# Kernel optimization log

Measured on AMD Instinct MI355X. Metric: run time of the kernel, lower is better.

The kernel has to match this reference:

```python
import jax, jax.numpy as jnp
import numpy as np

B, T, U = 4, 448, 448
SKS, BKS, H, V = 96, 32, 96, 128


def setup_inputs() -> dict:
    key = jax.random.key(0)
    ks = jax.random.split(key, 8)
    return {
        "s": jax.random.normal(ks[0], (B, T, SKS), jnp.float32),
        "b": jax.random.normal(ks[1], (B, U, BKS), jnp.float32),
        "W_sh": jax.random.normal(ks[2], (H, SKS), jnp.float32) * (1.0 / np.sqrt(SKS)),
        "b_sh": jax.random.normal(ks[3], (H,), jnp.float32) * 0.02,
        "W_bh": jax.random.normal(ks[4], (H, BKS), jnp.float32) * (1.0 / np.sqrt(BKS)),
        "b_bh": jax.random.normal(ks[5], (H,), jnp.float32) * 0.02,
        "W_out": jax.random.normal(ks[6], (V, H), jnp.float32) * (1.0 / np.sqrt(H)),
        "b_out": jax.random.normal(ks[7], (V,), jnp.float32) * 0.02,
    }


def reference(s, b, W_sh, b_sh, W_bh, b_bh, W_out, b_out):
    # input projections (self.sh / self.bh): [B,T,H] and [B,U,H]
    sh = jnp.einsum("bts,hs->bth", s, W_sh) + b_sh
    bh = jnp.einsum("buk,hk->buh", b, W_bh) + b_bh
    # broadcast outer-expand + relu gate: z[b,t,u,h] = sh[b,t,h] * relu(bh[b,u,h])
    z = sh[:, :, None, :] * jax.nn.relu(bh)[:, None, :, :]  # [B,T,U,H]
    # output projection (self.out) + log_softmax over vocab
    logits = jnp.einsum("btuh,vh->btuv", z, W_out) + b_out  # [B,T,U,V]
    return jax.nn.log_softmax(logits, axis=-1)
```

## Files before the change

kernel.cpp:

```cpp
#include <hip/hip_runtime.h>

#define B_ 4
#define T_ 448
#define U_ 448
#define SKS_ 96
#define BKS_ 32
#define H_ 96
#define V_ 128

typedef __attribute__((ext_vector_type(8))) short bf16x8;
typedef __attribute__((ext_vector_type(4))) float f32x4;
typedef __attribute__((ext_vector_type(4))) int i32x4;

__device__ __forceinline__ unsigned short f2bf(float f) {
    unsigned int u = __float_as_uint(f);
    u += 0x7fffu + ((u >> 16) & 1u);
    return (unsigned short)(u >> 16);
}
__device__ __forceinline__ float bf2f(unsigned short h) {
    return __uint_as_float(((unsigned int)h) << 16);
}

__global__ __launch_bounds__(128) void prep_kernel(
    const float* __restrict__ s, const float* __restrict__ b,
    const float* __restrict__ W_sh, const float* __restrict__ b_sh,
    const float* __restrict__ W_bh, const float* __restrict__ b_bh,
    const float* __restrict__ W_out,
    unsigned short* __restrict__ sh_ws,
    unsigned short* __restrict__ rbh_ws,
    unsigned short* __restrict__ w_ws)
{
    const int blk = blockIdx.x;
    const int tid = threadIdx.x;

    if (blk < B_ * T_) {
        __shared__ float row[SKS_];
        if (tid < SKS_) row[tid] = s[(size_t)blk * SKS_ + tid];
        __syncthreads();
        if (tid < H_) {
            const float* w = W_sh + (size_t)tid * SKS_;
            float acc = b_sh[tid];
            #pragma unroll
            for (int k = 0; k < SKS_; k += 4) {
                acc += row[k] * w[k] + row[k + 1] * w[k + 1]
                     + row[k + 2] * w[k + 2] + row[k + 3] * w[k + 3];
            }
            sh_ws[(size_t)blk * H_ + tid] = f2bf(acc);
        }
    } else if (blk < 2 * B_ * T_) {
        const int r = blk - B_ * T_;
        __shared__ float row2[BKS_];
        if (tid < BKS_) row2[tid] = b[(size_t)r * BKS_ + tid];
        __syncthreads();
        if (tid < H_) {
            const float* w = W_bh + (size_t)tid * BKS_;
            float acc = b_bh[tid];
            #pragma unroll
            for (int k = 0; k < BKS_; k += 4) {
                acc += row2[k] * w[k] + row2[k + 1] * w[k + 1]
                     + row2[k + 2] * w[k + 2] + row2[k + 3] * w[k + 3];
            }
            acc = fmaxf(acc, 0.0f);
            rbh_ws[(size_t)r * H_ + tid] = f2bf(acc);
        }
    } else {
        const int c = (blk - 2 * B_ * T_) * 128 + tid;
        const int k8 = c >> 7;
        const int n  = c & 127;
        const float* src = W_out + (size_t)n * H_ + k8 * 8;
        unsigned short tmp[8];
        #pragma unroll
        for (int j = 0; j < 8; j++) tmp[j] = f2bf(src[j]);
        i32x4 v;
        v.x = (int)((unsigned)tmp[0] | ((unsigned)tmp[1] << 16));
        v.y = (int)((unsigned)tmp[2] | ((unsigned)tmp[3] << 16));
        v.z = (int)((unsigned)tmp[4] | ((unsigned)tmp[5] << 16));
        v.w = (int)((unsigned)tmp[6] | ((unsigned)tmp[7] << 16));
        ((i32x4*)w_ws)[c] = v;
    }
}

__global__ __launch_bounds__(256) void joiner_kernel(
    const unsigned short* __restrict__ sh_ws,
    const unsigned short* __restrict__ rbh_ws,
    const unsigned short* __restrict__ w_ws,
    const float* __restrict__ b_out,
    float* __restrict__ out)
{
    __shared__ unsigned short Wl[12 * 128 * 8];
    __shared__ unsigned short Al[12 * 16 * 8];

    const int tid = threadIdx.x;
    const int u0  = blockIdx.x * 16;
    const int t0  = blockIdx.y * 4;
    const int bb  = blockIdx.z;

    {
        const i32x4* src = (const i32x4*)w_ws;
        i32x4* dst = (i32x4*)Wl;
        #pragma unroll
        for (int i = 0; i < 6; i++) {
            const int c = i * 256 + tid;
            dst[c] = src[c];
        }
    }
    if (tid < 192) {
        const int u  = tid & 15;
        const int k8 = tid >> 4;
        const i32x4* src = (const i32x4*)(rbh_ws +
            ((size_t)(bb * U_ + u0 + u)) * H_ + k8 * 8);
        ((i32x4*)Al)[tid] = *src;
    }
    __syncthreads();

    const int wave = tid >> 6;
    const int lane = tid & 63;
    const int t    = t0 + wave;
    const int n    = lane & 15;
    const int q    = lane >> 4;

    const unsigned short* shrow = sh_ws + ((size_t)(bb * T_ + t)) * H_;
    bf16x8 shf[3];
    #pragma unroll
    for (int ks = 0; ks < 3; ks++)
        shf[ks] = *(const bf16x8*)(shrow + ks * 32 + q * 8);

    f32x4 acc[8];
    #pragma unroll
    for (int nt = 0; nt < 8; nt++) acc[nt] = (f32x4){0.f, 0.f, 0.f, 0.f};

    #pragma unroll
    for (int ks = 0; ks < 3; ks++) {
        const bf16x8 rb = *(const bf16x8*)(Al + (ks * 64 + lane) * 8);
        bf16x8 af;
        #pragma unroll
        for (int j = 0; j < 8; j++) {
            const float z = bf2f((unsigned short)shf[ks][j]) *
                            bf2f((unsigned short)rb[j]);
            af[j] = (short)f2bf(z);
        }
        #pragma unroll
        for (int nt = 0; nt < 8; nt++) {
            const bf16x8 bfr = *(const bf16x8*)(Wl +
                ((size_t)((ks * 4 + q) * 128 + nt * 16 + n)) * 8);
            acc[nt] = __builtin_amdgcn_mfma_f32_16x16x32_bf16(af, bfr, acc[nt], 0, 0, 0);
        }
    }

    float bias[8];
    #pragma unroll
    for (int nt = 0; nt < 8; nt++) bias[nt] = b_out[nt * 16 + n];

    #pragma unroll
    for (int nt = 0; nt < 8; nt++) {
        #pragma unroll
        for (int r = 0; r < 4; r++) acc[nt][r] += bias[nt];
    }

    #pragma unroll
    for (int r = 0; r < 4; r++) {
        float m = acc[0][r];
        #pragma unroll
        for (int nt = 1; nt < 8; nt++) m = fmaxf(m, acc[nt][r]);
        #pragma unroll
        for (int sft = 1; sft <= 8; sft <<= 1)
            m = fmaxf(m, __shfl_xor(m, sft, 64));

        float ssum = 0.0f;
        #pragma unroll
        for (int nt = 0; nt < 8; nt++) ssum += __expf(acc[nt][r] - m);
        #pragma unroll
        for (int sft = 1; sft <= 8; sft <<= 1)
            ssum += __shfl_xor(ssum, sft, 64);

        const float logz = m + __logf(ssum);
        const int u_local = q * 4 + r;
        float* orow = out + (((size_t)(bb * T_ + t)) * U_ + (u0 + u_local)) * V_;
        #pragma unroll
        for (int nt = 0; nt < 8; nt++)
            orow[nt * 16 + n] = acc[nt][r] - logz;
    }
}

extern "C" void kernel_launch(void* const* d_in, const int* in_sizes, int n_in,
                              void* d_out, int out_size, void* d_ws, size_t ws_size,
                              hipStream_t stream)
{
    const float* s     = (const float*)d_in[0];
    const float* b     = (const float*)d_in[1];
    const float* W_sh  = (const float*)d_in[2];
    const float* b_sh  = (const float*)d_in[3];
    const float* W_bh  = (const float*)d_in[4];
    const float* b_bh  = (const float*)d_in[5];
    const float* W_out = (const float*)d_in[6];
    const float* b_out = (const float*)d_in[7];
    float* out = (float*)d_out;

    unsigned short* sh_ws  = (unsigned short*)d_ws;
    unsigned short* rbh_ws = sh_ws + (size_t)B_ * T_ * H_;
    unsigned short* w_ws   = rbh_ws + (size_t)B_ * U_ * H_;

    prep_kernel<<<2 * B_ * T_ + 12, 128, 0, stream>>>(
        s, b, W_sh, b_sh, W_bh, b_bh, W_out, sh_ws, rbh_ws, w_ws);

    joiner_kernel<<<dim3(U_ / 16, T_ / 4, B_), 256, 0, stream>>>(
        sh_ws, rbh_ws, w_ws, b_out, out);
}
```

Before: 425.8 us.

## Use MFMA for input projections and loop multiple t-rows per joiner block

```diff
diff --git a/kernel.cpp b/kernel.cpp
--- a/kernel.cpp
+++ b/kernel.cpp
@@ -20,8 +20,18 @@
 __device__ __forceinline__ float bf2f(unsigned short h) {
     return __uint_as_float(((unsigned int)h) << 16);
 }
-
-__global__ __launch_bounds__(128) void prep_kernel(
+__device__ __forceinline__ bf16x8 load_cvt8(const float* __restrict__ p) {
+    f32x4 a = *(const f32x4*)p;
+    f32x4 c = *(const f32x4*)(p + 4);
+    bf16x8 r;
+    r[0] = (short)f2bf(a.x); r[1] = (short)f2bf(a.y);
+    r[2] = (short)f2bf(a.z); r[3] = (short)f2bf(a.w);
+    r[4] = (short)f2bf(c.x); r[5] = (short)f2bf(c.y);
+    r[6] = (short)f2bf(c.z); r[7] = (short)f2bf(c.w);
+    return r;
+}
+
+__global__ __launch_bounds__(256) void prep_kernel(
     const float* __restrict__ s, const float* __restrict__ b,
     const float* __restrict__ W_sh, const float* __restrict__ b_sh,
     const float* __restrict__ W_bh, const float* __restrict__ b_bh,
@@ -30,44 +40,64 @@
     unsigned short* __restrict__ rbh_ws,
     unsigned short* __restrict__ w_ws)
 {
-    const int blk = blockIdx.x;
-    const int tid = threadIdx.x;
-
-    if (blk < B_ * T_) {
-        __shared__ float row[SKS_];
-        if (tid < SKS_) row[tid] = s[(size_t)blk * SKS_ + tid];
-        __syncthreads();
-        if (tid < H_) {
-            const float* w = W_sh + (size_t)tid * SKS_;
-            float acc = b_sh[tid];
-            #pragma unroll
-            for (int k = 0; k < SKS_; k += 4) {
-                acc += row[k] * w[k] + row[k + 1] * w[k + 1]
-                     + row[k + 2] * w[k + 2] + row[k + 3] * w[k + 3];
-            }
-            sh_ws[(size_t)blk * H_ + tid] = f2bf(acc);
-        }
-    } else if (blk < 2 * B_ * T_) {
-        const int r = blk - B_ * T_;
-        __shared__ float row2[BKS_];
-        if (tid < BKS_) row2[tid] = b[(size_t)r * BKS_ + tid];
-        __syncthreads();
-        if (tid < H_) {
-            const float* w = W_bh + (size_t)tid * BKS_;
-            float acc = b_bh[tid];
-            #pragma unroll
-            for (int k = 0; k < BKS_; k += 4) {
-                acc += row2[k] * w[k] + row2[k + 1] * w[k + 1]
-                     + row2[k + 2] * w[k + 2] + row2[k + 3] * w[k + 3];
-            }
-            acc = fmaxf(acc, 0.0f);
-            rbh_ws[(size_t)r * H_ + tid] = f2bf(acc);
+    const int blk  = blockIdx.x;
+    const int tid  = threadIdx.x;
+    const int wave = tid >> 6;
+    const int lane = tid & 63;
+    const int n    = lane & 15;
+    const int q    = lane >> 4;
+
+    if (blk < 28) {
+        const int row0 = blk * 64 + wave * 16;
+        bf16x8 af[3];
+        #pragma unroll
+        for (int ks = 0; ks < 3; ks++)
+            af[ks] = load_cvt8(s + (size_t)(row0 + n) * SKS_ + ks * 32 + q * 8);
+        f32x4 acc[6];
+        #pragma unroll
+        for (int nt = 0; nt < 6; nt++) acc[nt] = (f32x4){0.f, 0.f, 0.f, 0.f};
+        #pragma unroll
+        for (int ks = 0; ks < 3; ks++) {
+            #pragma unroll
+            for (int nt = 0; nt < 6; nt++) {
+                bf16x8 bf = load_cvt8(W_sh + (size_t)(nt * 16 + n) * SKS_ + ks * 32 + q * 8);
+                acc[nt] = __builtin_amdgcn_mfma_f32_16x16x32_bf16(af[ks], bf, acc[nt], 0, 0, 0);
+            }
+        }
+        #pragma unroll
+        for (int nt = 0; nt < 6; nt++) {
+            const float bias = b_sh[nt * 16 + n];
+            #pragma unroll
+            for (int r = 0; r < 4; r++) {
+                sh_ws[(size_t)(row0 + q * 4 + r) * H_ + nt * 16 + n] =
+                    f2bf(acc[nt][r] + bias);
+            }
+        }
+    } else if (blk < 56) {
+        const int row0 = (blk - 28) * 64 + wave * 16;
+        bf16x8 af = load_cvt8(b + (size_t)(row0 + n) * BKS_ + q * 8);
+        f32x4 acc[6];
+        #pragma unroll
+        for (int nt = 0; nt < 6; nt++) acc[nt] = (f32x4){0.f, 0.f, 0.f, 0.f};
+        #pragma unroll
+        for (int nt = 0; nt < 6; nt++) {
+            bf16x8 bf = load_cvt8(W_bh + (size_t)(nt * 16 + n) * BKS_ + q * 8);
+            acc[nt] = __builtin_amdgcn_mfma_f32_16x16x32_bf16(af, bf, acc[nt], 0, 0, 0);
+        }
+        #pragma unroll
+        for (int nt = 0; nt < 6; nt++) {
+            const float bias = b_bh[nt * 16 + n];
+            #pragma unroll
+            for (int r = 0; r < 4; r++) {
+                rbh_ws[(size_t)(row0 + q * 4 + r) * H_ + nt * 16 + n] =
+                    f2bf(fmaxf(acc[nt][r] + bias, 0.0f));
+            }
         }
     } else {
-        const int c = (blk - 2 * B_ * T_) * 128 + tid;
+        const int c = (blk - 56) * 256 + tid;
         const int k8 = c >> 7;
-        const int n  = c & 127;
-        const float* src = W_out + (size_t)n * H_ + k8 * 8;
+        const int n2 = c & 127;
+        const float* src = W_out + (size_t)n2 * H_ + k8 * 8;
         unsigned short tmp[8];
         #pragma unroll
         for (int j = 0; j < 8; j++) tmp[j] = f2bf(src[j]);
@@ -80,6 +110,7 @@
     }
 }
 
+#define TT_ 7
 __global__ __launch_bounds__(256) void joiner_kernel(
     const unsigned short* __restrict__ sh_ws,
     const unsigned short* __restrict__ rbh_ws,
@@ -88,11 +119,10 @@
     float* __restrict__ out)
 {
     __shared__ unsigned short Wl[12 * 128 * 8];
-    __shared__ unsigned short Al[12 * 16 * 8];
 
     const int tid = threadIdx.x;
     const int u0  = blockIdx.x * 16;
-    const int t0  = blockIdx.y * 4;
+    const int t0  = blockIdx.y * (4 * TT_);
     const int bb  = blockIdx.z;
 
     {
@@ -104,81 +134,82 @@
             dst[c] = src[c];
         }
     }
-    if (tid < 192) {
-        const int u  = tid & 15;
-        const int k8 = tid >> 4;
-        const i32x4* src = (const i32x4*)(rbh_ws +
-            ((size_t)(bb * U_ + u0 + u)) * H_ + k8 * 8);
-        ((i32x4*)Al)[tid] = *src;
-    }
     __syncthreads();
 
     const int wave = tid >> 6;
     const int lane = tid & 63;
-    const int t    = t0 + wave;
     const int n    = lane & 15;
     const int q    = lane >> 4;
 
-    const unsigned short* shrow = sh_ws + ((size_t)(bb * T_ + t)) * H_;
-    bf16x8 shf[3];
+    bf16x8 rb[3];
     #pragma unroll
     for (int ks = 0; ks < 3; ks++)
-        shf[ks] = *(const bf16x8*)(shrow + ks * 32 + q * 8);
-
-    f32x4 acc[8];
-    #pragma unroll
-    for (int nt = 0; nt < 8; nt++) acc[nt] = (f32x4){0.f, 0.f, 0.f, 0.f};
-
-    #pragma unroll
-    for (int ks = 0; ks < 3; ks++) {
-        const bf16x8 rb = *(const bf16x8*)(Al + (ks * 64 + lane) * 8);
-        bf16x8 af;
-        #pragma unroll
-        for (int j = 0; j < 8; j++) {
-            const float z = bf2f((unsigned short)shf[ks][j]) *
-                            bf2f((unsigned short)rb[j]);
-            af[j] = (short)f2bf(z);
-        }
-        #pragma unroll
-        for (int nt = 0; nt < 8; nt++) {
-            const bf16x8 bfr = *(const bf16x8*)(Wl +
-                ((size_t)((ks * 4 + q) * 128 + nt * 16 + n)) * 8);
-            acc[nt] = __builtin_amdgcn_mfma_f32_16x16x32_bf16(af, bfr, acc[nt], 0, 0, 0);
-        }
-    }
+        rb[ks] = *(const bf16x8*)(rbh_ws +
+            ((size_t)(bb * U_ + u0 + n)) * H_ + ks * 32 + q * 8);
 
     float bias[8];
     #pragma unroll
     for (int nt = 0; nt < 8; nt++) bias[nt] = b_out[nt * 16 + n];
 
-    #pragma unroll
-    for (int nt = 0; nt < 8; nt++) {
-        #pragma unroll
-        for (int r = 0; r < 4; r++) acc[nt][r] += bias[nt];
-    }
-
-    #pragma unroll
-    for (int r = 0; r < 4; r++) {
-        float m = acc[0][r];
-        #pragma unroll
-        for (int nt = 1; nt < 8; nt++) m = fmaxf(m, acc[nt][r]);
-        #pragma unroll
-        for (int sft = 1; sft <= 8; sft <<= 1)
-            m = fmaxf(m, __shfl_xor(m, sft, 64));
-
-        float ssum = 0.0f;
-        #pragma unroll
-        for (int nt = 0; nt < 8; nt++) ssum += __expf(acc[nt][r] - m);
-        #pragma unroll
-        for (int sft = 1; sft <= 8; sft <<= 1)
-            ssum += __shfl_xor(ssum, sft, 64);
-
-        const float logz = m + __logf(ssum);
-        const int u_local = q * 4 + r;
-        float* orow = out + (((size_t)(bb * T_ + t)) * U_ + (u0 + u_local)) * V_;
-        #pragma unroll
-        for (int nt = 0; nt < 8; nt++)
-            orow[nt * 16 + n] = acc[nt][r] - logz;
+    for (int i = 0; i < TT_; i++) {
+        const int t = t0 + i * 4 + wave;
+
+        const unsigned short* shrow = sh_ws + ((size_t)(bb * T_ + t)) * H_;
+        bf16x8 af[3];
+        #pragma unroll
+        for (int ks = 0; ks < 3; ks++) {
+            const bf16x8 sf = *(const bf16x8*)(shrow + ks * 32 + q * 8);
+            #pragma unroll
+            for (int j = 0; j < 8; j++) {
+                const float z = bf2f((unsigned short)sf[j]) *
+                                bf2f((unsigned short)rb[ks][j]);
+                af[ks][j] = (short)f2bf(z);
+            }
+        }
+
+        f32x4 acc[8];
+        #pragma unroll
+        for (int nt = 0; nt < 8; nt++) acc[nt] = (f32x4){0.f, 0.f, 0.f, 0.f};
+
+        #pragma unroll
+        for (int ks = 0; ks < 3; ks++) {
+            #pragma unroll
+            for (int nt = 0; nt < 8; nt++) {
+                const bf16x8 bfr = *(const bf16x8*)(Wl +
+                    ((size_t)((ks * 4 + q) * 128 + nt * 16 + n)) * 8);
+                acc[nt] = __builtin_amdgcn_mfma_f32_16x16x32_bf16(af[ks], bfr, acc[nt], 0, 0, 0);
+            }
+        }
+
+        #pragma unroll
+        for (int nt = 0; nt < 8; nt++) {
+            #pragma unroll
+            for (int r = 0; r < 4; r++) acc[nt][r] += bias[nt];
+        }
+
+        #pragma unroll
+        for (int r = 0; r < 4; r++) {
+            float m = acc[0][r];
+            #pragma unroll
+            for (int nt = 1; nt < 8; nt++) m = fmaxf(m, acc[nt][r]);
+            #pragma unroll
+            for (int sft = 1; sft <= 8; sft <<= 1)
+                m = fmaxf(m, __shfl_xor(m, sft, 64));
+
+            float ssum = 0.0f;
+            #pragma unroll
+            for (int nt = 0; nt < 8; nt++) ssum += __expf(acc[nt][r] - m);
+            #pragma unroll
+            for (int sft = 1; sft <= 8; sft <<= 1)
+                ssum += __shfl_xor(ssum, sft, 64);
+
+            const float logz = m + __logf(ssum);
+            const int u_local = q * 4 + r;
+            float* orow = out + (((size_t)(bb * T_ + t)) * U_ + (u0 + u_local)) * V_;
+            #pragma unroll
+            for (int nt = 0; nt < 8; nt++)
+                orow[nt * 16 + n] = acc[nt][r] - logz;
+        }
     }
 }
 
@@ -200,9 +231,9 @@
     unsigned short* rbh_ws = sh_ws + (size_t)B_ * T_ * H_;
     unsigned short* w_ws   = rbh_ws + (size_t)B_ * U_ * H_;
 
-    prep_kernel<<<2 * B_ * T_ + 12, 128, 0, stream>>>(
+    prep_kernel<<<62, 256, 0, stream>>>(
         s, b, W_sh, b_sh, W_bh, b_bh, W_out, sh_ws, rbh_ws, w_ws);
 
-    joiner_kernel<<<dim3(U_ / 16, T_ / 4, B_), 256, 0, stream>>>(
+    joiner_kernel<<<dim3(U_ / 16, T_ / (4 * TT_), B_), 256, 0, stream>>>(
         sh_ws, rbh_ws, w_ws, b_out, out);
 }
```

Result: slower. 451.7 us (+6.1%).
